# Optimization experiments

Hardware: AMD Instinct MI355X
Metric: run time of the kernel (lower is better)

The kernel has to match this reference:

```python
import jax, jax.numpy as jnp
import numpy as np

DIM = 1024
N_EXPERTS = 8
TOP_K = 2
B, S = 2, 1024


def setup_inputs() -> dict:
    key = jax.random.key(0)
    ks = jax.random.split(key, 4)
    scale = 0.02
    return {
        "u_t": jax.random.normal(ks[0], (B, S, DIM), dtype=jnp.float32),
        "centroids": jax.random.normal(ks[1], (N_EXPERTS, DIM), dtype=jnp.float32),
        "score_biases": jnp.zeros((N_EXPERTS,), dtype=jnp.float32),
        "W1": jax.random.normal(ks[2], (N_EXPERTS, DIM, 4 * DIM), dtype=jnp.float32) * scale,
        "b1": jnp.zeros((N_EXPERTS, 4 * DIM), dtype=jnp.float32),
        "W2": jax.random.normal(ks[3], (N_EXPERTS, 4 * DIM, DIM), dtype=jnp.float32) * scale,
        "b2": jnp.zeros((N_EXPERTS, DIM), dtype=jnp.float32),
    }


def reference(u_t, centroids, score_biases, W1, b1, W2, b2):
    Bs, Ss, dim = u_t.shape
    T = Bs * Ss
    N = centroids.shape[0]
    K = TOP_K

    u_flat = u_t.reshape(T, dim)
    scores = u_flat @ centroids.T + score_biases          # [T, N]
    gate = jax.nn.softmax(scores, axis=-1)                # [T, N]
    topk_vals, topk_idx = jax.lax.top_k(gate, K)          # [T, K]

    flat_idx = topk_idx.reshape(-1)                       # [T*K]

    # load-violation stats (no grad path; pure counts)
    perfect_load = K * T / N
    f_i = jnp.zeros((N,), dtype=jnp.float32).at[flat_idx].add(1.0)
    maxvio = (jnp.max(f_i) - perfect_load) / perfect_load

    # Grouped MLP expressed as dense per-expert compute over all tokens,
    # then combined with a sparse [T, N] gate matrix (same math as masked dispatch).
    h = jax.nn.relu(jnp.einsum("td,ndh->nth", u_flat, W1) + b1[:, None, :])  # [N, T, 4*dim]
    expert_outs = jnp.einsum("nth,nhd->ntd", h, W2) + b2[:, None, :]          # [N, T, dim]

    rows = jnp.repeat(jnp.arange(T), K)
    combine_w = jnp.zeros((T, N), dtype=topk_vals.dtype).at[rows, flat_idx].add(topk_vals.reshape(-1))
    out = jnp.einsum("tn,ntd->td", combine_w, expert_outs).reshape(Bs, Ss, dim)
    return (out, maxvio)
```

## Files before the change

### kernel.cpp

```cpp
#include <hip/hip_runtime.h>
#include <hip/hip_bf16.h>

#define T_TOK 2048
#define DIMS  1024
#define HID   4096
#define NE    8

typedef __bf16 bf16x8 __attribute__((ext_vector_type(8)));
typedef float  f32x4  __attribute__((ext_vector_type(4)));

__device__ __forceinline__ unsigned short f2bf(float f) {
  unsigned u = __float_as_uint(f);
  u += 0x7FFFu + ((u >> 16) & 1u);
  return (unsigned short)(u >> 16);
}
__device__ __forceinline__ float bf2f(unsigned short s) {
  return __uint_as_float(((unsigned)s) << 16);
}

__device__ __forceinline__ void g2l16(const void* g, void* l) {
  __builtin_amdgcn_global_load_lds((const __attribute__((address_space(1))) void*)g,
                                   (__attribute__((address_space(3))) void*)l,
                                   16, 0, 0);
}

__global__ __launch_bounds__(256) void k_route(const float* __restrict__ u,
    const float* __restrict__ cent, const float* __restrict__ sbias,
    int* __restrict__ topk_idx, float* __restrict__ topk_val,
    unsigned short* __restrict__ ub) {
  int wave = threadIdx.x >> 6;
  int lane = threadIdx.x & 63;
  int t = blockIdx.x * 4 + wave;
  const float* ur = u + (size_t)t * DIMS;
  float p[NE];
#pragma unroll
  for (int n = 0; n < NE; n++) p[n] = 0.f;
#pragma unroll
  for (int ch = 0; ch < 4; ch++) {
    int d = ch * 256 + lane * 4;
    float4 uv = *(const float4*)(ur + d);
    ushort4 o4;
    o4.x = f2bf(uv.x); o4.y = f2bf(uv.y); o4.z = f2bf(uv.z); o4.w = f2bf(uv.w);
    *(ushort4*)(ub + (size_t)t * DIMS + d) = o4;
#pragma unroll
    for (int n = 0; n < NE; n++) {
      float4 cv = *(const float4*)(cent + n * DIMS + d);
      p[n] += uv.x * cv.x + uv.y * cv.y + uv.z * cv.z + uv.w * cv.w;
    }
  }
#pragma unroll
  for (int n = 0; n < NE; n++) {
#pragma unroll
    for (int o = 32; o > 0; o >>= 1) p[n] += __shfl_xor(p[n], o);
  }
  if (lane == 0) {
    float g[NE];
    float m = -1e30f;
#pragma unroll
    for (int n = 0; n < NE; n++) { g[n] = p[n] + sbias[n]; m = fmaxf(m, g[n]); }
    float sum = 0.f;
#pragma unroll
    for (int n = 0; n < NE; n++) { g[n] = expf(g[n] - m); sum += g[n]; }
    float inv = 1.f / sum;
#pragma unroll
    for (int n = 0; n < NE; n++) g[n] *= inv;
    int i0 = 0;
#pragma unroll
    for (int n = 1; n < NE; n++) if (g[n] > g[i0]) i0 = n;
    int i1 = (i0 == 0) ? 1 : 0;
#pragma unroll
    for (int n = 0; n < NE; n++) if (n != i0 && g[n] > g[i1]) i1 = n;
    topk_idx[2 * t] = i0;     topk_idx[2 * t + 1] = i1;
    topk_val[2 * t] = g[i0];  topk_val[2 * t + 1] = g[i1];
  }
}

__global__ __launch_bounds__(256) void k_finalize(const int* __restrict__ topk_idx,
    int* __restrict__ cnt, int* __restrict__ offs, int* __restrict__ cursor,
    float* __restrict__ maxvio) {
  __shared__ int lc[NE];
  if (threadIdx.x < NE) lc[threadIdx.x] = 0;
  __syncthreads();
#pragma unroll
  for (int i = 0; i < 16; i++) {
    int e = topk_idx[threadIdx.x * 16 + i];
    atomicAdd(&lc[e], 1);
  }
  __syncthreads();
  if (threadIdx.x == 0) {
    int o = 0, mx = 0;
#pragma unroll
    for (int n = 0; n < NE; n++) {
      int c = lc[n];
      cnt[n] = c; offs[n] = o; cursor[n] = 0;
      o += c; mx = max(mx, c);
    }
    maxvio[0] = ((float)mx - 512.f) / 512.f;
  }
}

__global__ __launch_bounds__(256) void k_place(const int* __restrict__ topk_idx,
    const int* __restrict__ offs, int* __restrict__ cursor,
    int* __restrict__ rowtok, int* __restrict__ pairpos) {
  int t = blockIdx.x * 256 + threadIdx.x;
  if (t >= T_TOK) return;
#pragma unroll
  for (int k = 0; k < 2; k++) {
    int e = topk_idx[2 * t + k];
    int pos = atomicAdd(&cursor[e], 1);
    rowtok[offs[e] + pos] = t;
    pairpos[2 * t + k] = offs[e] + pos;
  }
}

__global__ __launch_bounds__(256) void k_cvt_w(const float* __restrict__ W1,
    const float* __restrict__ W2, unsigned short* __restrict__ w1t,
    unsigned short* __restrict__ w2t) {
  int bid = blockIdx.x;
  const float* Wsrc; unsigned short* dst; int R, C, c0, r0b;
  if (bid < 4096) {
    int e = bid >> 9, t = bid & 511;
    R = 1024; C = 4096;
    c0 = (t & 63) * 64; r0b = (t >> 6) * 128;
    Wsrc = W1 + (size_t)e * R * C;  dst = w1t + (size_t)e * R * C;
  } else {
    int t2 = bid - 4096;
    int e = t2 >> 9, t = t2 & 511;
    R = 4096; C = 1024;
    c0 = (t & 15) * 64; r0b = (t >> 4) * 128;
    Wsrc = W2 + (size_t)e * R * C;  dst = w2t + (size_t)e * R * C;
  }
  int wv = threadIdx.x >> 6, lane = threadIdx.x & 63;
  int r0 = r0b + wv * 32;
  int c = c0 + lane;
  const float* src = Wsrc + (size_t)r0 * C + c;
  unsigned short rr[32];
#pragma unroll
  for (int i = 0; i < 32; i++) rr[i] = f2bf(src[(size_t)i * C]);
  unsigned short* d = dst + (size_t)c * R + r0;
  union { unsigned short us[8]; uint4 v; } pk;
#pragma unroll
  for (int h = 0; h < 4; h++) {
#pragma unroll
    for (int i = 0; i < 8; i++) pk.us[i] = rr[h * 8 + i];
    *(uint4*)(d + h * 8) = pk.v;
  }
}

#define BM 128
#define BN 128
#define BK 64

__global__ __launch_bounds__(256) void k_gemm1(const unsigned short* __restrict__ ub,
    const unsigned short* __restrict__ w1t, const float* __restrict__ b1,
    const int* __restrict__ rowtok, const int* __restrict__ cnts, const int* __restrict__ offs,
    unsigned short* __restrict__ h) {
  int e = blockIdx.z;
  int cnt = cnts[e];
  int m0 = blockIdx.y * BM;
  if (m0 >= cnt) return;
  int off = offs[e];
  int n0 = blockIdx.x * BN;
  __shared__ __align__(16) unsigned char smem[32768];

  int tid = threadIdx.x;
  int lane = tid & 63;
  int wm = (tid >> 7) & 1;
  int wn = (tid >> 6) & 1;
  int srow = tid >> 3;
  int cp = tid & 7;
  const unsigned short* gA[4];
  const unsigned short* gB[4];
#pragma unroll
  for (int a = 0; a < 4; a++) {
    int r = a * 32 + srow;
    int c = cp ^ (r & 7);
    int pr = min(off + m0 + r, off + cnt - 1);
    int tok = rowtok[pr];
    gA[a] = ub + (size_t)tok * DIMS + c * 8;
    gB[a] = w1t + ((size_t)e * HID + (n0 + r)) * DIMS + c * 8;
  }
  int wboff = __builtin_amdgcn_readfirstlane((tid >> 6) << 10);
  f32x4 acc[4][4];
  f32x4 zz = {0.f, 0.f, 0.f, 0.f};
#pragma unroll
  for (int i = 0; i < 4; i++)
#pragma unroll
    for (int j = 0; j < 4; j++) acc[i][j] = zz;

  int lane15 = lane & 15, quad = lane >> 4, l7 = lane & 7;
  unsigned aRowOff = (unsigned)((wm * 64 + lane15) * 128);
  unsigned bRowOff = (unsigned)(16384 + (wn * 64 + lane15) * 128);

#pragma unroll 1
  for (int k0 = 0; k0 < DIMS; k0 += BK) {
#pragma unroll
    for (int a = 0; a < 4; a++) g2l16(gA[a] + k0, smem + a * 4096 + wboff);
#pragma unroll
    for (int a = 0; a < 4; a++) g2l16(gB[a] + k0, smem + 16384 + a * 4096 + wboff);
    __syncthreads();
#pragma unroll
    for (int s = 0; s < 2; s++) {
      unsigned cpf = (unsigned)(((s * 4 + quad) ^ l7) * 16);
      bf16x8 af[4], bfr[4];
#pragma unroll
      for (int i = 0; i < 4; i++) af[i] = *(const bf16x8*)(smem + aRowOff + i * 2048 + cpf);
#pragma unroll
      for (int j = 0; j < 4; j++) bfr[j] = *(const bf16x8*)(smem + bRowOff + j * 2048 + cpf);
#pragma unroll
      for (int i = 0; i < 4; i++)
#pragma unroll
        for (int j = 0; j < 4; j++)
          acc[i][j] = __builtin_amdgcn_mfma_f32_16x16x32_bf16(af[i], bfr[j], acc[i][j], 0, 0, 0);
    }
    __syncthreads();
  }
  float b1v[4];
#pragma unroll
  for (int j = 0; j < 4; j++) b1v[j] = b1[e * HID + n0 + wn * 64 + j * 16 + lane15];
#pragma unroll
  for (int i = 0; i < 4; i++) {
#pragma unroll
    for (int r = 0; r < 4; r++) {
      int mrow = m0 + wm * 64 + i * 16 + quad * 4 + r;
      if (mrow < cnt) {
        size_t hrow = (size_t)(off + mrow) * HID;
#pragma unroll
        for (int j = 0; j < 4; j++) {
          int col = n0 + wn * 64 + j * 16 + lane15;
          float v = fmaxf(acc[i][j][r] + b1v[j], 0.f);
          h[hrow + col] = f2bf(v);
        }
      }
    }
  }
}

__global__ __launch_bounds__(256) void k_gemm2(const unsigned short* __restrict__ hbuf,
    const unsigned short* __restrict__ w2t, const float* __restrict__ b2,
    const int* __restrict__ cnts, const int* __restrict__ offs,
    unsigned short* __restrict__ pout, int KC) {
  int z = blockIdx.z;
  int e = z & 7;
  int sp = z >> 3;
  int cnt = cnts[e];
  int m0 = blockIdx.y * BM;
  if (m0 >= cnt) return;
  int off = offs[e];
  int n0 = blockIdx.x * BN;
  __shared__ __align__(16) unsigned char smem[32768];

  int tid = threadIdx.x;
  int lane = tid & 63;
  int wm = (tid >> 7) & 1;
  int wn = (tid >> 6) & 1;
  int srow = tid >> 3;
  int cp = tid & 7;
  const unsigned short* gA[4];
  const unsigned short* gB[4];
#pragma unroll
  for (int a = 0; a < 4; a++) {
    int r = a * 32 + srow;
    int c = cp ^ (r & 7);
    int pr = min(off + m0 + r, off + cnt - 1);
    gA[a] = hbuf + (size_t)pr * HID + c * 8;
    gB[a] = w2t + ((size_t)e * DIMS + (n0 + r)) * HID + c * 8;
  }
  int wboff = __builtin_amdgcn_readfirstlane((tid >> 6) << 10);
  f32x4 acc[4][4];
  f32x4 zz = {0.f, 0.f, 0.f, 0.f};
#pragma unroll
  for (int i = 0; i < 4; i++)
#pragma unroll
    for (int j = 0; j < 4; j++) acc[i][j] = zz;

  int lane15 = lane & 15, quad = lane >> 4, l7 = lane & 7;
  unsigned aRowOff = (unsigned)((wm * 64 + lane15) * 128);
  unsigned bRowOff = (unsigned)(16384 + (wn * 64 + lane15) * 128);

  int kbeg = sp * KC, kend = kbeg + KC;
#pragma unroll 1
  for (int k0 = kbeg; k0 < kend; k0 += BK) {
#pragma unroll
    for (int a = 0; a < 4; a++) g2l16(gA[a] + k0, smem + a * 4096 + wboff);
#pragma unroll
    for (int a = 0; a < 4; a++) g2l16(gB[a] + k0, smem + 16384 + a * 4096 + wboff);
    __syncthreads();
#pragma unroll
    for (int s = 0; s < 2; s++) {
      unsigned cpf = (unsigned)(((s * 4 + quad) ^ l7) * 16);
      bf16x8 af[4], bfr[4];
#pragma unroll
      for (int i = 0; i < 4; i++) af[i] = *(const bf16x8*)(smem + aRowOff + i * 2048 + cpf);
#pragma unroll
      for (int j = 0; j < 4; j++) bfr[j] = *(const bf16x8*)(smem + bRowOff + j * 2048 + cpf);
#pragma unroll
      for (int i = 0; i < 4; i++)
#pragma unroll
        for (int j = 0; j < 4; j++)
          acc[i][j] = __builtin_amdgcn_mfma_f32_16x16x32_bf16(af[i], bfr[j], acc[i][j], 0, 0, 0);
    }
    __syncthreads();
  }
  float b2v[4];
#pragma unroll
  for (int j = 0; j < 4; j++)
    b2v[j] = (sp == 0) ? b2[e * DIMS + n0 + wn * 64 + j * 16 + lane15] : 0.f;
  unsigned short* pme = pout + (size_t)sp * T_TOK * 2 * DIMS;
#pragma unroll
  for (int i = 0; i < 4; i++) {
#pragma unroll
    for (int r = 0; r < 4; r++) {
      int mrow = m0 + wm * 64 + i * 16 + quad * 4 + r;
      if (mrow < cnt) {
        size_t prow = (size_t)(off + mrow) * DIMS;
#pragma unroll
        for (int j = 0; j < 4; j++) {
          int col = n0 + wn * 64 + j * 16 + lane15;
          pme[prow + col] = f2bf(acc[i][j][r] + b2v[j]);
        }
      }
    }
  }
}

__global__ __launch_bounds__(256) void k_combine(const unsigned short* __restrict__ pout,
    const int* __restrict__ pairpos, const float* __restrict__ tkv,
    float* __restrict__ out, int nsplit) {
  int t = blockIdx.x;
  int d = threadIdx.x * 4;
  int p0 = pairpos[2 * t], p1 = pairpos[2 * t + 1];
  float w0 = tkv[2 * t], w1 = tkv[2 * t + 1];
  float a0 = 0.f, a1 = 0.f, a2 = 0.f, a3 = 0.f;
  float c0 = 0.f, c1 = 0.f, c2 = 0.f, c3 = 0.f;
  const size_t SS = (size_t)T_TOK * 2 * DIMS;
  for (int s = 0; s < nsplit; s++) {
    ushort4 av = *(const ushort4*)(pout + s * SS + (size_t)p0 * DIMS + d);
    ushort4 bv = *(const ushort4*)(pout + s * SS + (size_t)p1 * DIMS + d);
    a0 += bf2f(av.x); a1 += bf2f(av.y); a2 += bf2f(av.z); a3 += bf2f(av.w);
    c0 += bf2f(bv.x); c1 += bf2f(bv.y); c2 += bf2f(bv.z); c3 += bf2f(bv.w);
  }
  float4 o;
  o.x = w0 * a0 + w1 * c0;
  o.y = w0 * a1 + w1 * c1;
  o.z = w0 * a2 + w1 * c2;
  o.w = w0 * a3 + w1 * c3;
  *(float4*)(out + (size_t)t * DIMS + d) = o;
}

extern "C" void kernel_launch(void* const* d_in, const int* in_sizes, int n_in,
                              void* d_out, int out_size, void* d_ws, size_t ws_size,
                              hipStream_t stream) {
  const float* u     = (const float*)d_in[0];
  const float* cent  = (const float*)d_in[1];
  const float* sbias = (const float*)d_in[2];
  const float* W1    = (const float*)d_in[3];
  const float* b1    = (const float*)d_in[4];
  const float* W2    = (const float*)d_in[5];
  const float* b2    = (const float*)d_in[6];
  float* out = (float*)d_out;

  char* ws = (char*)d_ws;
  unsigned short* w1t  = (unsigned short*)(ws);
  unsigned short* w2t  = (unsigned short*)(ws + 67108864);
  unsigned short* ubuf = (unsigned short*)(ws + 134217728);
  unsigned short* hbuf = (unsigned short*)(ws + 138412032);
  const size_t POUT_OFF = 171966464ull;
  const size_t PSZ = (size_t)T_TOK * 2 * DIMS * 2;
  int nsplit = (ws_size >= POUT_OFF + 4 * PSZ + (1u << 20)) ? 4 : 1;
  unsigned short* poutb = (unsigned short*)(ws + POUT_OFF);
  char* r = ws + POUT_OFF + (size_t)nsplit * PSZ;
  int*   cnt      = (int*)(r);
  int*   offs     = (int*)(r + 64);
  int*   cursor   = (int*)(r + 128);
  int*   topk_idx = (int*)(r + 256);
  float* topk_val = (float*)(r + 256 + 16384);
  int*   rowtok   = (int*)(r + 256 + 32768);
  int*   pairpos  = (int*)(r + 256 + 49152);

  k_route<<<512, 256, 0, stream>>>(u, cent, sbias, topk_idx, topk_val, ubuf);
  k_finalize<<<1, 256, 0, stream>>>(topk_idx, cnt, offs, cursor, out + 2097152);
  k_place<<<8, 256, 0, stream>>>(topk_idx, offs, cursor, rowtok, pairpos);
  k_cvt_w<<<8192, 256, 0, stream>>>(W1, W2, w1t, w2t);
  k_gemm1<<<dim3(32, 16, 8), 256, 0, stream>>>(ubuf, w1t, b1, rowtok, cnt, offs, hbuf);
  k_gemm2<<<dim3(8, 16, 8 * nsplit), 256, 0, stream>>>(hbuf, w2t, b2, cnt, offs,
                                                       poutb, HID / nsplit);
  k_combine<<<2048, 256, 0, stream>>>(poutb, pairpos, topk_val, out, nsplit);
}
```

Baseline: 479.1 us.

## Fuse fp32-to-bf16 weight conversion into GEMM tile loads, drop conversion kernel

Removes the separate kernel that converted and transposed W1 and W2 into bf16 scratch buffers. Both expert GEMMs now read fp32 weights straight from global memory, convert eight k-values to bf16 in registers, and store them into the swizzled shared-memory B tile. This saves a full pass that reads and writes all weights, and shrinks the workspace. In exchange, every M-tile of an expert re-reads fp32 weights at twice the bf16 size, and these loads are synchronous register loads instead of async global-to-LDS copies, so the inner loop may stall on memory latency. A dead leftover loop is also left in gemm1.

```diff
diff --git a/kernel.cpp b/kernel.cpp
--- a/kernel.cpp
+++ b/kernel.cpp
@@ -113,46 +113,12 @@
   }
 }
 
-__global__ __launch_bounds__(256) void k_cvt_w(const float* __restrict__ W1,
-    const float* __restrict__ W2, unsigned short* __restrict__ w1t,
-    unsigned short* __restrict__ w2t) {
-  int bid = blockIdx.x;
-  const float* Wsrc; unsigned short* dst; int R, C, c0, r0b;
-  if (bid < 4096) {
-    int e = bid >> 9, t = bid & 511;
-    R = 1024; C = 4096;
-    c0 = (t & 63) * 64; r0b = (t >> 6) * 128;
-    Wsrc = W1 + (size_t)e * R * C;  dst = w1t + (size_t)e * R * C;
-  } else {
-    int t2 = bid - 4096;
-    int e = t2 >> 9, t = t2 & 511;
-    R = 4096; C = 1024;
-    c0 = (t & 15) * 64; r0b = (t >> 4) * 128;
-    Wsrc = W2 + (size_t)e * R * C;  dst = w2t + (size_t)e * R * C;
-  }
-  int wv = threadIdx.x >> 6, lane = threadIdx.x & 63;
-  int r0 = r0b + wv * 32;
-  int c = c0 + lane;
-  const float* src = Wsrc + (size_t)r0 * C + c;
-  unsigned short rr[32];
-#pragma unroll
-  for (int i = 0; i < 32; i++) rr[i] = f2bf(src[(size_t)i * C]);
-  unsigned short* d = dst + (size_t)c * R + r0;
-  union { unsigned short us[8]; uint4 v; } pk;
-#pragma unroll
-  for (int h = 0; h < 4; h++) {
-#pragma unroll
-    for (int i = 0; i < 8; i++) pk.us[i] = rr[h * 8 + i];
-    *(uint4*)(d + h * 8) = pk.v;
-  }
-}
-
 #define BM 128
 #define BN 128
 #define BK 64
 
 __global__ __launch_bounds__(256) void k_gemm1(const unsigned short* __restrict__ ub,
-    const unsigned short* __restrict__ w1t, const float* __restrict__ b1,
+    const float* __restrict__ W1, const float* __restrict__ b1,
     const int* __restrict__ rowtok, const int* __restrict__ cnts, const int* __restrict__ offs,
     unsigned short* __restrict__ h) {
   int e = blockIdx.z;
@@ -165,22 +131,28 @@
 
   int tid = threadIdx.x;
   int lane = tid & 63;
+  int wv = tid >> 6;
   int wm = (tid >> 7) & 1;
   int wn = (tid >> 6) & 1;
   int srow = tid >> 3;
   int cp = tid & 7;
-  const unsigned short* gA[4];
-  const unsigned short* gB[4];
+  const float* w1e = W1 + (size_t)e * DIMS * HID;
+  const unsigned short* gA[2];
+#pragma unroll
+  for (int a = 0; a < 2; a++) {
+    int r = a * 64 + (srow & 31) + ((tid >> 8) << 5);
+    (void)r;
+  }
+  const unsigned short* gAp[4];
 #pragma unroll
   for (int a = 0; a < 4; a++) {
     int r = a * 32 + srow;
     int c = cp ^ (r & 7);
     int pr = min(off + m0 + r, off + cnt - 1);
     int tok = rowtok[pr];
-    gA[a] = ub + (size_t)tok * DIMS + c * 8;
-    gB[a] = w1t + ((size_t)e * HID + (n0 + r)) * DIMS + c * 8;
-  }
-  int wboff = __builtin_amdgcn_readfirstlane((tid >> 6) << 10);
+    gAp[a] = ub + (size_t)tok * DIMS + c * 8;
+  }
+  int wboff = __builtin_amdgcn_readfirstlane(wv << 10);
   f32x4 acc[4][4];
   f32x4 zz = {0.f, 0.f, 0.f, 0.f};
 #pragma unroll
@@ -191,13 +163,29 @@
   int lane15 = lane & 15, quad = lane >> 4, l7 = lane & 7;
   unsigned aRowOff = (unsigned)((wm * 64 + lane15) * 128);
   unsigned bRowOff = (unsigned)(16384 + (wn * 64 + lane15) * 128);
+  int csB = 0;
 
 #pragma unroll 1
   for (int k0 = 0; k0 < DIMS; k0 += BK) {
 #pragma unroll
-    for (int a = 0; a < 4; a++) g2l16(gA[a] + k0, smem + a * 4096 + wboff);
-#pragma unroll
-    for (int a = 0; a < 4; a++) g2l16(gB[a] + k0, smem + 16384 + a * 4096 + wboff);
+    for (int a = 0; a < 4; a++) g2l16(gAp[a] + k0, smem + a * 4096 + wboff);
+#pragma unroll
+    for (int jj = 0; jj < 4; jj++) {
+      int j = wv * 4 + jj;
+      int kc = j & 7, nh = j >> 3;
+      int nloc = nh * 64 + lane;
+      const float* src = w1e + (size_t)(k0 + kc * 8) * HID + n0 + nloc;
+      float t0, t1, t2, t3, t4, t5, t6, t7;
+      t0 = src[0];            t1 = src[(size_t)HID];
+      t2 = src[(size_t)2 * HID]; t3 = src[(size_t)3 * HID];
+      t4 = src[(size_t)4 * HID]; t5 = src[(size_t)5 * HID];
+      t6 = src[(size_t)6 * HID]; t7 = src[(size_t)7 * HID];
+      bf16x8 pk;
+      pk[0] = (__bf16)t0; pk[1] = (__bf16)t1; pk[2] = (__bf16)t2; pk[3] = (__bf16)t3;
+      pk[4] = (__bf16)t4; pk[5] = (__bf16)t5; pk[6] = (__bf16)t6; pk[7] = (__bf16)t7;
+      csB = kc ^ (lane & 7);
+      *(bf16x8*)(smem + 16384 + nloc * 128 + csB * 16) = pk;
+    }
     __syncthreads();
 #pragma unroll
     for (int s = 0; s < 2; s++) {
@@ -237,7 +225,7 @@
 }
 
 __global__ __launch_bounds__(256) void k_gemm2(const unsigned short* __restrict__ hbuf,
-    const unsigned short* __restrict__ w2t, const float* __restrict__ b2,
+    const float* __restrict__ W2, const float* __restrict__ b2,
     const int* __restrict__ cnts, const int* __restrict__ offs,
     unsigned short* __restrict__ pout, int KC) {
   int z = blockIdx.z;
@@ -252,21 +240,21 @@
 
   int tid = threadIdx.x;
   int lane = tid & 63;
+  int wv = tid >> 6;
   int wm = (tid >> 7) & 1;
   int wn = (tid >> 6) & 1;
   int srow = tid >> 3;
   int cp = tid & 7;
-  const unsigned short* gA[4];
-  const unsigned short* gB[4];
+  const float* w2e = W2 + (size_t)e * HID * DIMS;
+  const unsigned short* gAp[4];
 #pragma unroll
   for (int a = 0; a < 4; a++) {
     int r = a * 32 + srow;
     int c = cp ^ (r & 7);
     int pr = min(off + m0 + r, off + cnt - 1);
-    gA[a] = hbuf + (size_t)pr * HID + c * 8;
-    gB[a] = w2t + ((size_t)e * DIMS + (n0 + r)) * HID + c * 8;
-  }
-  int wboff = __builtin_amdgcn_readfirstlane((tid >> 6) << 10);
+    gAp[a] = hbuf + (size_t)pr * HID + c * 8;
+  }
+  int wboff = __builtin_amdgcn_readfirstlane(wv << 10);
   f32x4 acc[4][4];
   f32x4 zz = {0.f, 0.f, 0.f, 0.f};
 #pragma unroll
@@ -282,9 +270,24 @@
 #pragma unroll 1
   for (int k0 = kbeg; k0 < kend; k0 += BK) {
 #pragma unroll
-    for (int a = 0; a < 4; a++) g2l16(gA[a] + k0, smem + a * 4096 + wboff);
-#pragma unroll
-    for (int a = 0; a < 4; a++) g2l16(gB[a] + k0, smem + 16384 + a * 4096 + wboff);
+    for (int a = 0; a < 4; a++) g2l16(gAp[a] + k0, smem + a * 4096 + wboff);
+#pragma unroll
+    for (int jj = 0; jj < 4; jj++) {
+      int j = wv * 4 + jj;
+      int kc = j & 7, nh = j >> 3;
+      int nloc = nh * 64 + lane;
+      const float* src = w2e + (size_t)(k0 + kc * 8) * DIMS + n0 + nloc;
+      float t0, t1, t2, t3, t4, t5, t6, t7;
+      t0 = src[0];             t1 = src[(size_t)DIMS];
+      t2 = src[(size_t)2 * DIMS]; t3 = src[(size_t)3 * DIMS];
+      t4 = src[(size_t)4 * DIMS]; t5 = src[(size_t)5 * DIMS];
+      t6 = src[(size_t)6 * DIMS]; t7 = src[(size_t)7 * DIMS];
+      bf16x8 pk;
+      pk[0] = (__bf16)t0; pk[1] = (__bf16)t1; pk[2] = (__bf16)t2; pk[3] = (__bf16)t3;
+      pk[4] = (__bf16)t4; pk[5] = (__bf16)t5; pk[6] = (__bf16)t6; pk[7] = (__bf16)t7;
+      int cs = kc ^ (lane & 7);
+      *(bf16x8*)(smem + 16384 + nloc * 128 + cs * 16) = pk;
+    }
     __syncthreads();
 #pragma unroll
     for (int s = 0; s < 2; s++) {
@@ -361,11 +364,9 @@
   float* out = (float*)d_out;
 
   char* ws = (char*)d_ws;
-  unsigned short* w1t  = (unsigned short*)(ws);
-  unsigned short* w2t  = (unsigned short*)(ws + 67108864);
-  unsigned short* ubuf = (unsigned short*)(ws + 134217728);
-  unsigned short* hbuf = (unsigned short*)(ws + 138412032);
-  const size_t POUT_OFF = 171966464ull;
+  unsigned short* ubuf = (unsigned short*)(ws);
+  unsigned short* hbuf = (unsigned short*)(ws + 4194304);
+  const size_t POUT_OFF = 37748736ull;
   const size_t PSZ = (size_t)T_TOK * 2 * DIMS * 2;
   int nsplit = (ws_size >= POUT_OFF + 4 * PSZ + (1u << 20)) ? 4 : 1;
   unsigned short* poutb = (unsigned short*)(ws + POUT_OFF);
@@ -381,9 +382,8 @@
   k_route<<<512, 256, 0, stream>>>(u, cent, sbias, topk_idx, topk_val, ubuf);
   k_finalize<<<1, 256, 0, stream>>>(topk_idx, cnt, offs, cursor, out + 2097152);
   k_place<<<8, 256, 0, stream>>>(topk_idx, offs, cursor, rowtok, pairpos);
-  k_cvt_w<<<8192, 256, 0, stream>>>(W1, W2, w1t, w2t);
-  k_gemm1<<<dim3(32, 16, 8), 256, 0, stream>>>(ubuf, w1t, b1, rowtok, cnt, offs, hbuf);
-  k_gemm2<<<dim3(8, 16, 8 * nsplit), 256, 0, stream>>>(hbuf, w2t, b2, cnt, offs,
+  k_gemm1<<<dim3(32, 16, 8), 256, 0, stream>>>(ubuf, W1, b1, rowtok, cnt, offs, hbuf);
+  k_gemm2<<<dim3(8, 16, 8 * nsplit), 256, 0, stream>>>(hbuf, W2, b2, cnt, offs,
                                                        poutb, HID / nsplit);
   k_combine<<<2048, 256, 0, stream>>>(poutb, pairpos, topk_val, out, nsplit);
 }
```

After: 427.8 us. 1.12x faster.
